# Kernel optimization log

Measured on AMD Instinct MI355X. Metric: run time of the kernel, lower is better.

## Reference

```python
import jax, jax.numpy as jnp
import numpy as np

PI = 3.141592653589793
N, B, DIM, HEADS = 4, 8192, 1024, 4
HD = DIM // HEADS  # head_dim = 256


def setup_inputs() -> dict:
    key = jax.random.key(0)
    ks = jax.random.split(key, 10)
    glorot = jax.nn.initializers.glorot_uniform()
    return {
        "axis_embeddings": jax.random.normal(ks[0], (N, B, DIM), jnp.float32),
        "arg_embeddings": jax.random.uniform(ks[1], (N, B, DIM), jnp.float32),
        "W_axis1": glorot(ks[2], (HD, 2 * HD), jnp.float32),
        "b_axis1": jnp.zeros((HD,), jnp.float32),
        "W_arg1": glorot(ks[3], (HD, 2 * HD), jnp.float32),
        "b_arg1": jnp.zeros((HD,), jnp.float32),
        "W_axis2": glorot(ks[4], (HD, HD), jnp.float32),
        "b_axis2": jnp.zeros((HD,), jnp.float32),
        "W_arg2": glorot(ks[5], (HD, HD), jnp.float32),
        "b_arg2": jnp.zeros((HD,), jnp.float32),
    }


def _linear(x, W, b):
    return jnp.einsum('...i,oi->...o', x, W) + b


def reference(axis_embeddings, arg_embeddings, W_axis1, b_axis1, W_arg1, b_arg1,
              W_axis2, b_axis2, W_arg2, b_arg2):
    axis = axis_embeddings.reshape(N, B, HEADS, HD)
    arg = arg_embeddings.reshape(N, B, HEADS, HD)
    al = axis - arg / 2
    ah = axis + arg / 2
    logits = jnp.concatenate([al, ah], axis=-1)  # [N,B,H,2*HD]

    # axis branch: attention over N then circular mean via atan2-style correction
    axis_h1 = jax.nn.relu(_linear(logits, W_axis1, b_axis1))
    axis_attn = jax.nn.softmax(_linear(axis_h1, W_axis2, b_axis2), axis=0)
    x_emb = jnp.sum(axis_attn * jnp.cos(axis), axis=0)  # [B,H,HD]
    y_emb = jnp.sum(axis_attn * jnp.sin(axis), axis=0)
    x_emb = jnp.where(jnp.abs(x_emb) < 0.001, 0.001, x_emb)
    axis_out = jnp.arctan(y_emb / x_emb)
    ind_x = x_emb < 0
    ind_y = y_emb < 0
    ind_two = ind_x & jnp.logical_not(ind_y)
    ind_three = ind_x & ind_y
    axis_out = axis_out + PI * ind_two.astype(axis_out.dtype) - PI * ind_three.astype(axis_out.dtype)

    # arg branch: mean-pooled gate, min over N (dropout p=0 -> identity)
    arg_h1 = jax.nn.relu(_linear(logits, W_arg1, b_arg1))
    gate = jax.nn.sigmoid(_linear(jnp.mean(arg_h1, axis=0), W_arg2, b_arg2))
    arg_out = jnp.min(arg, axis=0) * gate

    return axis_out.reshape(B, DIM), arg_out.reshape(B, DIM)
```

## Files before the change

kernel.cpp:

```cpp
#include <hip/hip_runtime.h>


typedef __attribute__((ext_vector_type(8))) _Float16 f16x8;
typedef __attribute__((ext_vector_type(8))) float f32x8;
typedef __attribute__((ext_vector_type(4))) float f32x4;
typedef __attribute__((ext_vector_type(16))) float f32x16;

#define BH 32768
#define OUT_ARG_OFF 8388608

#define O_WXA_H 0
#define O_WXA_L 65536
#define O_WXR_H 131072
#define O_WXR_L 196608
#define O_WRA_H 262144
#define O_WRR_H 327680
#define O_W2X_H 393216
#define O_W2X_L 458752
#define O_W2G_H 524288
#define WS_HALFS 589824

__device__ __forceinline__ void split16(float x, _Float16& hi, _Float16& lo) {
  float xs = x * 16.0f;
  _Float16 h = (_Float16)xs;
  hi = h;
  lo = (_Float16)(xs - (float)h);
}

__device__ __forceinline__ int fragidx16(int o, int k) {
  return ((o >> 4) * 8 + (k >> 5)) * 512 + ((((k >> 3) & 3) << 4) + (o & 15)) * 8 + (k & 7);
}
__device__ __forceinline__ int fragidx32(int o, int k) {
  return ((o >> 5) * 16 + (k >> 4)) * 512 + ((((k >> 3) & 1) << 5) + (o & 31)) * 8 + (k & 7);
}

__global__ void combine_weights(const float* __restrict__ Wx1, const float* __restrict__ Wr1,
                                const float* __restrict__ W2x, const float* __restrict__ W2g,
                                _Float16* __restrict__ ws) {
  int i = blockIdx.x * 256 + threadIdx.x;
  int o = i >> 8, k = i & 255;
  int d = fragidx32(o, k);
  float a = Wx1[o * 512 + k], b = Wx1[o * 512 + 256 + k];
  _Float16 h, l;
  split16(a + b, h, l);          ws[O_WXA_H + d] = h; ws[O_WXA_L + d] = l;
  split16(0.5f * (b - a), h, l); ws[O_WXR_H + d] = h; ws[O_WXR_L + d] = l;
  a = Wr1[o * 512 + k]; b = Wr1[o * 512 + 256 + k];
  ws[O_WRA_H + d] = (_Float16)((a + b) * 16.0f);
  ws[O_WRR_H + d] = (_Float16)((0.5f * (b - a)) * 16.0f);
  split16(W2x[o * 256 + k], h, l); ws[O_W2X_H + d] = h; ws[O_W2X_L + d] = l;
  ws[O_W2G_H + fragidx16(o, k)] = (_Float16)(W2g[o * 256 + k] * 16.0f);
}

#define MFMA16 __builtin_amdgcn_mfma_f32_16x16x32_f16
#define MFMA32 __builtin_amdgcn_mfma_f32_32x32x16_f16

__device__ __forceinline__ void gemm1_pass32(const _Float16* __restrict__ ws,
                                             int oBh, int oBl, int oBm,
                                             const _Float16* bufH, const _Float16* bufL,
                                             int w, int l,
                                             f32x16& acc1, f32x16& accm) {
  const int row = l & 31;
  const int hi8 = (l >> 5) << 3;
  f16x8 wh[2], wl[2], wm[2];
  {
    const int fb = (w * 16) * 512 + l * 8;
    wh[0] = *(const f16x8*)(ws + oBh + fb);
    wl[0] = *(const f16x8*)(ws + oBl + fb);
    wm[0] = *(const f16x8*)(ws + oBm + fb);
  }
  #pragma unroll
  for (int st = 0; st < 16; ++st) {
    const int cur = st & 1, nx = cur ^ 1;
    if (st < 15) {
      const int fb = (w * 16 + st + 1) * 512 + l * 8;
      wh[nx] = *(const f16x8*)(ws + oBh + fb);
      wl[nx] = *(const f16x8*)(ws + oBl + fb);
      wm[nx] = *(const f16x8*)(ws + oBm + fb);
    }
    const int ad = row * 256 + ((st * 16 + hi8) ^ ((row & 31) << 3));
    const f16x8 ah = *(const f16x8*)(bufH + ad);
    const f16x8 al = *(const f16x8*)(bufL + ad);
    __builtin_amdgcn_s_setprio(1);
    acc1 = MFMA32(ah, wh[cur], acc1, 0, 0, 0);
    acc1 = MFMA32(al, wh[cur], acc1, 0, 0, 0);
    acc1 = MFMA32(ah, wl[cur], acc1, 0, 0, 0);
    accm = MFMA32(ah, wm[cur], accm, 0, 0, 0);
    __builtin_amdgcn_s_setprio(0);
  }
}

__global__ __launch_bounds__(512, 2)
void cone_main(const float* __restrict__ axisF, const float* __restrict__ argF,
               const float* __restrict__ bx1, const float* __restrict__ br1,
               const float* __restrict__ bg2,
               const _Float16* __restrict__ ws, float* __restrict__ out)
{
  __shared__ __align__(16) _Float16 lds[32768];
  _Float16* bufAxH = lds;
  _Float16* bufAxL = lds + 8192;
  _Float16* bufArH = lds + 16384;
  _Float16* bufArL = lds + 24576;

  const int tid = threadIdx.x;
  const int w   = tid >> 6;
  const int l   = tid & 63;
  const int l15 = l & 15;
  const int lg  = l >> 4;
  const int l31 = l & 31;
  const int lh  = l >> 5;
  int bid = blockIdx.x;
  bid = ((bid & 7) << 9) + (bid >> 3);
  const int g0 = bid << 3;
  const float s = 1.0f / 256.0f;

  {
    #pragma unroll
    for (int c = 0; c < 2; ++c) {
      const int i   = c * 512 + tid;
      const int row = i >> 5;
      const int col = (i & 31) * 8;
      const int gofs = ((row & 3) * BH + g0 + (row >> 2)) * 256 + col;
      f32x8 va = *(const f32x8*)(axisF + gofs);
      f32x8 vr = *(const f32x8*)(argF + gofs);
      f16x8 xh, xl, rh, rl;
      #pragma unroll
      for (int j = 0; j < 8; ++j) {
        _Float16 h, lo2;
        split16(va[j], h, lo2); xh[j] = h; xl[j] = lo2;
        split16(vr[j], h, lo2); rh[j] = h; rl[j] = lo2;
      }
      const int ad = row * 256 + (col ^ ((row & 31) << 3));
      *(f16x8*)(bufAxH + ad) = xh;
      *(f16x8*)(bufAxL + ad) = xl;
      *(f16x8*)(bufArH + ad) = rh;
      *(f16x8*)(bufArL + ad) = rl;
    }
  }
  __syncthreads();

  f32x16 acc1, accm;
  #pragma unroll
  for (int i = 0; i < 16; ++i) { acc1[i] = 0.f; accm[i] = 0.f; }

  gemm1_pass32(ws, O_WXA_H, O_WXA_L, O_WRA_H, bufAxH, bufAxL, w, l, acc1, accm);
  gemm1_pass32(ws, O_WXR_H, O_WXR_L, O_WRR_H, bufArH, bufArL, w, l, acc1, accm);
  __syncthreads();

  _Float16* h1h = bufAxH;
  _Float16* h1l = bufAxL;
  _Float16* h1m = bufArH;
  *(unsigned long long*)&h1m[2048 + tid * 4] = 0ull;
  {
    const int c = (w << 5) + l31;
    const float bvx = bx1[c];
    const float bvr = br1[c];
    #pragma unroll
    for (int g = 0; g < 4; ++g) {
      float sm = 0.f;
      #pragma unroll
      for (int n = 0; n < 4; ++n) {
        const int r = g * 4 + n;
        const int row = (r & 3) + 8 * (r >> 2) + 4 * lh;
        const float v = fmaxf(acc1[r] * s + bvx, 0.f);
        _Float16 h, lo2; split16(v, h, lo2);
        const int ad = row * 256 + (c ^ ((row & 31) << 3));
        h1h[ad] = h; h1l[ad] = lo2;
        sm += fmaxf(accm[r] * s + bvr, 0.f);
      }
      const int p = 2 * g + lh;
      h1m[p * 256 + (c ^ ((p & 7) << 3))] = (_Float16)(0.25f * sm * 16.0f);
    }
  }
  __syncthreads();

  f32x16 acc2;
  #pragma unroll
  for (int i = 0; i < 16; ++i) acc2[i] = 0.f;
  {
    const int row = l31;
    const int hi8 = lh << 3;
    f16x8 w2h[2], w2l[2];
    {
      const int fb = (w * 16) * 512 + l * 8;
      w2h[0] = *(const f16x8*)(ws + O_W2X_H + fb);
      w2l[0] = *(const f16x8*)(ws + O_W2X_L + fb);
    }
    #pragma unroll
    for (int st = 0; st < 16; ++st) {
      const int cur = st & 1, nx = cur ^ 1;
      if (st < 15) {
        const int fb = (w * 16 + st + 1) * 512 + l * 8;
        w2h[nx] = *(const f16x8*)(ws + O_W2X_H + fb);
        w2l[nx] = *(const f16x8*)(ws + O_W2X_L + fb);
      }
      const int ad = row * 256 + ((st * 16 + hi8) ^ ((row & 31) << 3));
      const f16x8 ah = *(const f16x8*)(h1h + ad);
      const f16x8 al = *(const f16x8*)(h1l + ad);
      __builtin_amdgcn_s_setprio(1);
      acc2 = MFMA32(ah, w2h[cur], acc2, 0, 0, 0);
      acc2 = MFMA32(al, w2h[cur], acc2, 0, 0, 0);
      acc2 = MFMA32(ah, w2l[cur], acc2, 0, 0, 0);
      __builtin_amdgcn_s_setprio(0);
    }
  }

  f32x4 acc3[2];
  acc3[0] = (f32x4){0, 0, 0, 0}; acc3[1] = (f32x4){0, 0, 0, 0};
  {
    f16x8 wg[2][2];
    #pragma unroll
    for (int nt = 0; nt < 2; ++nt)
      wg[0][nt] = *(const f16x8*)(ws + O_W2G_H + (((w << 1) + nt) << 3) * 512 + l * 8);
    #pragma unroll
    for (int kk = 0; kk < 8; ++kk) {
      const int cur = kk & 1, nx = cur ^ 1;
      if (kk < 7) {
        #pragma unroll
        for (int nt = 0; nt < 2; ++nt)
          wg[nx][nt] = *(const f16x8*)(ws + O_W2G_H + ((((w << 1) + nt) << 3) + kk + 1) * 512 + l * 8);
      }
      const int k0 = (kk << 5) + (lg << 3);
      const f16x8 am = *(const f16x8*)&h1m[l15 * 256 + (k0 ^ ((l15 & 7) << 3))];
      acc3[0] = MFMA16(am, wg[cur][0], acc3[0], 0, 0, 0);
      acc3[1] = MFMA16(am, wg[cur][1], acc3[1], 0, 0, 0);
    }
  }

  {
    const int c = (w << 5) + l31;
    float av[4][4];
    #pragma unroll
    for (int g = 0; g < 4; ++g) {
      const int gi = g0 + 2 * g + lh;
      #pragma unroll
      for (int n = 0; n < 4; ++n) av[g][n] = axisF[(n * BH + gi) * 256 + c];
    }
    #pragma unroll
    for (int g = 0; g < 4; ++g) {
      float lv[4];
      #pragma unroll
      for (int n = 0; n < 4; ++n) lv[n] = acc2[g * 4 + n] * s;
      const float mx = fmaxf(fmaxf(lv[0], lv[1]), fmaxf(lv[2], lv[3]));
      float e[4]; float sum = 0.f;
      #pragma unroll
      for (int n = 0; n < 4; ++n) { e[n] = __expf(lv[n] - mx); sum += e[n]; }
      const float inv = 1.f / sum;
      float x = 0.f, y = 0.f;
      #pragma unroll
      for (int n = 0; n < 4; ++n) {
        float sn, cs2;
        __sincosf(av[g][n], &sn, &cs2);
        const float at = e[n] * inv;
        x += at * cs2;
        y += at * sn;
      }
      if (fabsf(x) < 0.001f) x = 0.001f;
      const int gi = g0 + 2 * g + lh;
      out[gi * 256 + c] = atan2f(y, x);
    }
  }

  {
    #pragma unroll
    for (int nt = 0; nt < 2; ++nt) {
      const int c = (w << 5) + (nt << 4) + l15;
      const float bgv = bg2[c];
      float ag[4][4];
      #pragma unroll
      for (int r = 0; r < 4; ++r) {
        const int p = (lg << 2) + r;
        if (p < 8) {
          const int gi = g0 + p;
          #pragma unroll
          for (int n = 0; n < 4; ++n) ag[r][n] = argF[(n * BH + gi) * 256 + c];
        }
      }
      #pragma unroll
      for (int r = 0; r < 4; ++r) {
        const int p = (lg << 2) + r;
        if (p < 8) {
          const int gi = g0 + p;
          const float gate = 1.f / (1.f + __expf(-(acc3[nt][r] * s + bgv)));
          const float mn = fminf(fminf(ag[r][0], ag[r][1]), fminf(ag[r][2], ag[r][3]));
          out[OUT_ARG_OFF + gi * 256 + c] = mn * gate;
        }
      }
    }
  }
}

extern "C" void kernel_launch(void* const* d_in, const int* in_sizes, int n_in,
                              void* d_out, int out_size, void* d_ws, size_t ws_size,
                              hipStream_t stream) {
  const float* axisF = (const float*)d_in[0];
  const float* argF  = (const float*)d_in[1];
  const float* Wx1   = (const float*)d_in[2];
  const float* bx1   = (const float*)d_in[3];
  const float* Wr1   = (const float*)d_in[4];
  const float* br1   = (const float*)d_in[5];
  const float* W2x   = (const float*)d_in[6];
  const float* W2g   = (const float*)d_in[8];
  const float* bg2   = (const float*)d_in[9];
  float* out = (float*)d_out;
  _Float16* ws = (_Float16*)d_ws;

  combine_weights<<<256, 256, 0, stream>>>(Wx1, Wr1, W2x, W2g, ws);
  cone_main<<<4096, 512, 0, stream>>>(axisF, argF, bx1, br1, bg2, ws, out);
}
```

Before: 288.1 us.

## Stage axis and arg inputs sequentially to shrink LDS and raise occupancy

The axis and arg tiles are no longer staged into LDS together. They are staged one at a time into a single shared hi/lo buffer pair, with a GEMM pass run after each. This cuts the shared-memory footprint from 64KB to 40KB and raises the launch-bounds occupancy hint from 2 to 4 blocks per CU. The trade-off is two extra block barriers and serialized load/GEMM phases. The tighter register budget implied by 4 blocks of 512 threads could also force spills.

```diff
diff --git a/kernel.cpp b/kernel.cpp
--- a/kernel.cpp
+++ b/kernel.cpp
@@ -54,6 +54,24 @@
 #define MFMA16 __builtin_amdgcn_mfma_f32_16x16x32_f16
 #define MFMA32 __builtin_amdgcn_mfma_f32_32x32x16_f16
 
+__device__ __forceinline__ void stage32(const float* __restrict__ src, int g0, int tid,
+                                        _Float16* bufH, _Float16* bufL) {
+  #pragma unroll
+  for (int c = 0; c < 2; ++c) {
+    const int i   = c * 512 + tid;
+    const int row = i >> 5;
+    const int col = (i & 31) * 8;
+    const int gofs = ((row & 3) * BH + g0 + (row >> 2)) * 256 + col;
+    f32x8 v = *(const f32x8*)(src + gofs);
+    f16x8 xh, xl;
+    #pragma unroll
+    for (int j = 0; j < 8; ++j) { _Float16 h, lo2; split16(v[j], h, lo2); xh[j] = h; xl[j] = lo2; }
+    const int ad = row * 256 + (col ^ ((row & 31) << 3));
+    *(f16x8*)(bufH + ad) = xh;
+    *(f16x8*)(bufL + ad) = xl;
+  }
+}
+
 __device__ __forceinline__ void gemm1_pass32(const _Float16* __restrict__ ws,
                                              int oBh, int oBl, int oBm,
                                              const _Float16* bufH, const _Float16* bufL,
@@ -89,17 +107,16 @@
   }
 }
 
-__global__ __launch_bounds__(512, 2)
+__global__ __launch_bounds__(512, 4)
 void cone_main(const float* __restrict__ axisF, const float* __restrict__ argF,
                const float* __restrict__ bx1, const float* __restrict__ br1,
                const float* __restrict__ bg2,
                const _Float16* __restrict__ ws, float* __restrict__ out)
 {
-  __shared__ __align__(16) _Float16 lds[32768];
-  _Float16* bufAxH = lds;
-  _Float16* bufAxL = lds + 8192;
-  _Float16* bufArH = lds + 16384;
-  _Float16* bufArL = lds + 24576;
+  __shared__ __align__(16) _Float16 lds[20480];
+  _Float16* bufH = lds;
+  _Float16* bufL = lds + 8192;
+  _Float16* h1m  = lds + 16384;
 
   const int tid = threadIdx.x;
   const int w   = tid >> 6;
@@ -113,42 +130,22 @@
   const int g0 = bid << 3;
   const float s = 1.0f / 256.0f;
 
-  {
-    #pragma unroll
-    for (int c = 0; c < 2; ++c) {
-      const int i   = c * 512 + tid;
-      const int row = i >> 5;
-      const int col = (i & 31) * 8;
-      const int gofs = ((row & 3) * BH + g0 + (row >> 2)) * 256 + col;
-      f32x8 va = *(const f32x8*)(axisF + gofs);
-      f32x8 vr = *(const f32x8*)(argF + gofs);
-      f16x8 xh, xl, rh, rl;
-      #pragma unroll
-      for (int j = 0; j < 8; ++j) {
-        _Float16 h, lo2;
-        split16(va[j], h, lo2); xh[j] = h; xl[j] = lo2;
-        split16(vr[j], h, lo2); rh[j] = h; rl[j] = lo2;
-      }
-      const int ad = row * 256 + (col ^ ((row & 31) << 3));
-      *(f16x8*)(bufAxH + ad) = xh;
-      *(f16x8*)(bufAxL + ad) = xl;
-      *(f16x8*)(bufArH + ad) = rh;
-      *(f16x8*)(bufArL + ad) = rl;
-    }
-  }
-  __syncthreads();
-
   f32x16 acc1, accm;
   #pragma unroll
   for (int i = 0; i < 16; ++i) { acc1[i] = 0.f; accm[i] = 0.f; }
 
-  gemm1_pass32(ws, O_WXA_H, O_WXA_L, O_WRA_H, bufAxH, bufAxL, w, l, acc1, accm);
-  gemm1_pass32(ws, O_WXR_H, O_WXR_L, O_WRR_H, bufArH, bufArL, w, l, acc1, accm);
-  __syncthreads();
-
-  _Float16* h1h = bufAxH;
-  _Float16* h1l = bufAxL;
-  _Float16* h1m = bufArH;
+  stage32(axisF, g0, tid, bufH, bufL);
+  __syncthreads();
+  gemm1_pass32(ws, O_WXA_H, O_WXA_L, O_WRA_H, bufH, bufL, w, l, acc1, accm);
+  __syncthreads();
+
+  stage32(argF, g0, tid, bufH, bufL);
+  __syncthreads();
+  gemm1_pass32(ws, O_WXR_H, O_WXR_L, O_WRR_H, bufH, bufL, w, l, acc1, accm);
+  __syncthreads();
+
+  _Float16* h1h = bufH;
+  _Float16* h1l = bufL;
   *(unsigned long long*)&h1m[2048 + tid * 4] = 0ull;
   {
     const int c = (w << 5) + l31;
```

Result: no change. 292.2 us (+1.4%).
